# Kernel tuning notes

Measured on AMD Instinct MI355X. Metric: run time of the kernel, lower is better.

The kernel has to match this reference:

```python
import jax, jax.numpy as jnp
import numpy as np

B, H, L, DK, DV = 4, 16, 1024, 64, 64

def setup_inputs() -> dict:
    key = jax.random.key(0)
    k1, k2, k3, k4 = jax.random.split(key, 4)
    Q = jax.random.normal(k1, (B, H, L, DK), dtype=jnp.float32)
    K = jax.random.normal(k2, (B, H, L, DK), dtype=jnp.float32)
    V = jax.random.normal(k3, (B, H, L, DV), dtype=jnp.float32)
    attn_mask = jax.random.randint(k4, (B, H, L, L), 0, 2).astype(jnp.bool_)
    return {"Q": Q, "K": K, "V": V, "attn_mask": attn_mask}

def reference(Q, K, V, attn_mask):
    # NOTE: original torch code uses d_k = Q.size(1) == n_heads (a bug kept for fidelity)
    scale = 1.0 / jnp.sqrt(jnp.asarray(Q.shape[1], dtype=Q.dtype))
    scores = jnp.einsum('bhqd,bhkd->bhqk', Q, K) * scale
    scores = jnp.where(attn_mask, jnp.asarray(-1e9, dtype=scores.dtype), scores)
    attn = jax.nn.softmax(scores, axis=-1)
    context = jnp.einsum('bhqk,bhkv->bhqv', attn, V)
    return (context, attn)
```

## Files before the change

### kernel.cpp

```cpp
#include <hip/hip_runtime.h>
#include <hip/hip_bf16.h>

typedef _Float16 half8 __attribute__((ext_vector_type(8)));
typedef _Float16 half2v __attribute__((ext_vector_type(2)));
typedef __fp16 fp16x2 __attribute__((ext_vector_type(2)));
typedef float f32x4 __attribute__((ext_vector_type(4)));
typedef int i32x4 __attribute__((ext_vector_type(4)));

#define BH_ 64
#define L_ 1024
#define DK_ 64

__device__ __forceinline__ unsigned short f2h(float f) {
    _Float16 h = (_Float16)f;
    return __builtin_bit_cast(unsigned short, h);
}
__device__ __forceinline__ unsigned int pk2h(float a, float b) {
    fp16x2 h = __builtin_amdgcn_cvt_pkrtz(a, b);
    return __builtin_bit_cast(unsigned int, h);
}

template<int OFF>
__device__ __forceinline__ void gl_h8(half8& d, const unsigned short* p) {
    asm volatile("global_load_dwordx4 %0, %1, off offset:%2"
                 : "=&v"(d) : "v"(p), "n"(OFF));
}
template<int OFF>
__device__ __forceinline__ void gl_i4(i32x4& d, const int* p) {
    asm volatile("global_load_dwordx4 %0, %1, off offset:%2"
                 : "=&v"(d) : "v"(p), "n"(OFF));
}
template<int OFF>
__device__ __forceinline__ void gl_f4(f32x4& d, const float* p) {
    asm volatile("global_load_dwordx4 %0, %1, off offset:%2"
                 : "=&v"(d) : "v"(p), "n"(OFF));
}
template<int N>
__device__ __forceinline__ void wait_vm() {
    asm volatile("s_waitcnt vmcnt(%0)" :: "n"(N) : "memory");
    __builtin_amdgcn_sched_barrier(0);
}

__global__ void prep_k(const float* __restrict__ K, unsigned short* __restrict__ Kh) {
    int idx = blockIdx.x * 256 + threadIdx.x;
    float4 v = reinterpret_cast<const float4*>(K)[idx];
    ushort4 o;
    o.x = f2h(v.x); o.y = f2h(v.y); o.z = f2h(v.z); o.w = f2h(v.w);
    reinterpret_cast<ushort4*>(Kh)[idx] = o;
}

__global__ void prep_v(const float* __restrict__ V, unsigned short* __restrict__ Vt) {
    __shared__ float lds[64][65];
    int bh = blockIdx.x >> 4, kt = blockIdx.x & 15;
    int t = threadIdx.x;
    const float* Vb = V + ((size_t)bh * L_ + kt * 64) * DK_;
#pragma unroll
    for (int it = 0; it < 4; ++it) {
        int idx = it * 256 + t;
        int row = idx >> 4, c4 = idx & 15;
        float4 v = reinterpret_cast<const float4*>(Vb + (size_t)row * DK_)[c4];
        lds[row][c4 * 4 + 0] = v.x; lds[row][c4 * 4 + 1] = v.y;
        lds[row][c4 * 4 + 2] = v.z; lds[row][c4 * 4 + 3] = v.w;
    }
    __syncthreads();
    unsigned short* Vtb = Vt + (size_t)bh * 64 * L_ + kt * 64;
#pragma unroll
    for (int it = 0; it < 4; ++it) {
        int idx = it * 256 + t;
        int n = idx >> 4, c4 = idx & 15;
        ushort4 o;
        o.x = f2h(lds[c4 * 4 + 0][n]);
        o.y = f2h(lds[c4 * 4 + 1][n]);
        o.z = f2h(lds[c4 * 4 + 2][n]);
        o.w = f2h(lds[c4 * 4 + 3][n]);
        *reinterpret_cast<ushort4*>(Vtb + (size_t)n * L_ + c4 * 4) = o;
    }
}

__global__ __launch_bounds__(256, 3) void attn_main(
    const float* __restrict__ Q, const int* __restrict__ mask,
    const unsigned short* __restrict__ Kh, const unsigned short* __restrict__ Vt,
    float* __restrict__ ctx_out, float* __restrict__ attn_out)
{
    const int qt = blockIdx.x, bh = blockIdx.y;
    const int tid = threadIdx.x;
    const int w = tid >> 6;
    const int lane = tid & 63;
    const int lg = lane >> 4, lr = lane & 15;
    const int q0 = qt * 16;

    __shared__ float red[2][4][16];
    __shared__ union {
        unsigned short pbuf[4][640];
        float ctxbuf[4][16][68];
    } u;

    const size_t rowbase = ((size_t)bh * L_ + q0 + lr) * L_;
    const float* qp = Q + ((size_t)bh * L_ + q0 + lr) * DK_ + lg * 8;
    const int* mp = mask + rowbase + w * 256 + lg * 4;
    const unsigned short* kp = Kh + ((size_t)bh * L_ + w * 256 + lr) * DK_ + lg * 8;

    i32x4 mreg[16];
#define LM(T) gl_i4<(T) * 64>(mreg[T], mp)
    LM(0); LM(1); LM(2); LM(3); LM(4); LM(5); LM(6); LM(7);
    LM(8); LM(9); LM(10); LM(11); LM(12); LM(13); LM(14); LM(15);
#undef LM
    f32x4 qf0, qf1, qf2, qf3;
    gl_f4<0>(qf0, qp); gl_f4<16>(qf1, qp);
    gl_f4<128>(qf2, qp); gl_f4<144>(qf3, qp);

    half8 ka[2][4], kb[2][4];
#define ISSUE_K(BUF, C) { \
    const unsigned short* a0_ = kp + (C) * 4096; \
    const unsigned short* a2_ = a0_ + 2048; \
    gl_h8<0>(ka[BUF][0], a0_);    gl_h8<64>(kb[BUF][0], a0_); \
    gl_h8<2048>(ka[BUF][1], a0_); gl_h8<2112>(kb[BUF][1], a0_); \
    gl_h8<0>(ka[BUF][2], a2_);    gl_h8<64>(kb[BUF][2], a2_); \
    gl_h8<2048>(ka[BUF][3], a2_); gl_h8<2112>(kb[BUF][3], a2_); }
    ISSUE_K(0, 0);

    wait_vm<12>();
    unsigned int mw0 = 0, mw1 = 0;
#pragma unroll
    for (int t = 0; t < 8; ++t) {
        mw0 |= (unsigned(mreg[t][0] != 0) << (t * 4 + 0))
             | (unsigned(mreg[t][1] != 0) << (t * 4 + 1))
             | (unsigned(mreg[t][2] != 0) << (t * 4 + 2))
             | (unsigned(mreg[t][3] != 0) << (t * 4 + 3));
        mw1 |= (unsigned(mreg[t + 8][0] != 0) << (t * 4 + 0))
             | (unsigned(mreg[t + 8][1] != 0) << (t * 4 + 1))
             | (unsigned(mreg[t + 8][2] != 0) << (t * 4 + 2))
             | (unsigned(mreg[t + 8][3] != 0) << (t * 4 + 3));
    }

    wait_vm<8>();
    half8 qh[2];
#pragma unroll
    for (int j = 0; j < 4; ++j) {
        qh[0][j]     = (_Float16)qf0[j];
        qh[0][j + 4] = (_Float16)qf1[j];
        qh[1][j]     = (_Float16)qf2[j];
        qh[1][j + 4] = (_Float16)qf3[j];
    }

    ISSUE_K(1, 1);

    unsigned int sh[16][2];
    float mx = -INFINITY;
#define QK_TILE(BUF, T, TT) { \
    f32x4 acc_ = {0.f, 0.f, 0.f, 0.f}; \
    acc_ = __builtin_amdgcn_mfma_f32_16x16x32_f16(ka[BUF][T], qh[0], acc_, 0, 0, 0); \
    acc_ = __builtin_amdgcn_mfma_f32_16x16x32_f16(kb[BUF][T], qh[1], acc_, 0, 0, 0); \
    const unsigned int word_ = ((TT) < 8) ? mw0 : mw1; \
    float s0_ = ((word_ >> (((TT) & 7) * 4 + 0)) & 1u) ? -INFINITY : 0.25f * acc_[0]; \
    float s1_ = ((word_ >> (((TT) & 7) * 4 + 1)) & 1u) ? -INFINITY : 0.25f * acc_[1]; \
    float s2_ = ((word_ >> (((TT) & 7) * 4 + 2)) & 1u) ? -INFINITY : 0.25f * acc_[2]; \
    float s3_ = ((word_ >> (((TT) & 7) * 4 + 3)) & 1u) ? -INFINITY : 0.25f * acc_[3]; \
    sh[TT][0] = pk2h(s0_, s1_); sh[TT][1] = pk2h(s2_, s3_); \
    mx = fmaxf(mx, fmaxf(fmaxf(s0_, s1_), fmaxf(s2_, s3_))); }

    wait_vm<8>();
    QK_TILE(0, 0, 0); QK_TILE(0, 1, 1); QK_TILE(0, 2, 2); QK_TILE(0, 3, 3);
    ISSUE_K(0, 2);
    wait_vm<8>();
    QK_TILE(1, 0, 4); QK_TILE(1, 1, 5); QK_TILE(1, 2, 6); QK_TILE(1, 3, 7);
    ISSUE_K(1, 3);
    wait_vm<8>();
    QK_TILE(0, 0, 8); QK_TILE(0, 1, 9); QK_TILE(0, 2, 10); QK_TILE(0, 3, 11);
    wait_vm<0>();
    QK_TILE(1, 0, 12); QK_TILE(1, 1, 13); QK_TILE(1, 2, 14); QK_TILE(1, 3, 15);

    mx = fmaxf(mx, __shfl_xor(mx, 16));
    mx = fmaxf(mx, __shfl_xor(mx, 32));
    if (lane < 16) red[0][w][lr] = mx;
    __syncthreads();
    const float gm = fmaxf(fmaxf(red[0][0][lr], red[0][1][lr]),
                           fmaxf(red[0][2][lr], red[0][3][lr]));

    float lsum = 0.f;
#pragma unroll
    for (int tt = 0; tt < 16; ++tt) {
        half2v a = __builtin_bit_cast(half2v, sh[tt][0]);
        half2v b = __builtin_bit_cast(half2v, sh[tt][1]);
        float p0 = __expf((float)a[0] - gm);
        float p1 = __expf((float)a[1] - gm);
        float p2 = __expf((float)b[0] - gm);
        float p3 = __expf((float)b[1] - gm);
        lsum += (p0 + p1) + (p2 + p3);
        sh[tt][0] = pk2h(p0, p1);
        sh[tt][1] = pk2h(p2, p3);
    }
    lsum += __shfl_xor(lsum, 16);
    lsum += __shfl_xor(lsum, 32);
    if (lane < 16) red[1][w][lr] = lsum;
    __syncthreads();
    const float gsum = red[1][0][lr] + red[1][1][lr] + red[1][2][lr] + red[1][3][lr];
    const float rinv = 1.0f / gsum;

    const unsigned short* vp = Vt + ((size_t)bh * 64 + lr) * L_ + w * 256 + lg * 8;
    f32x4 cacc[4] = {{0,0,0,0},{0,0,0,0},{0,0,0,0},{0,0,0,0}};
    unsigned short* pb = &u.pbuf[w][0];
    half8 vv[2][2][4];
#define ISSUE_V(BUF, C) { \
    const unsigned short* b0_ = vp + (C) * 32; \
    const unsigned short* b1_ = b0_ + 16384; \
    const unsigned short* b2_ = b0_ + 32768; \
    const unsigned short* b3_ = b0_ + 49152; \
    gl_h8<0>(vv[BUF][0][0], b0_); gl_h8<64>(vv[BUF][1][0], b0_); \
    gl_h8<0>(vv[BUF][0][1], b1_); gl_h8<64>(vv[BUF][1][1], b1_); \
    gl_h8<0>(vv[BUF][0][2], b2_); gl_h8<64>(vv[BUF][1][2], b2_); \
    gl_h8<0>(vv[BUF][0][3], b3_); gl_h8<64>(vv[BUF][1][3], b3_); }
#define PV_C(BUF, H, C) { \
    uint2 pr0_; pr0_.x = sh[2 * (C)][0]; pr0_.y = sh[2 * (C)][1]; \
    *reinterpret_cast<uint2*>(&pb[lr * 40 + lg * 4]) = pr0_; \
    uint2 pr1_; pr1_.x = sh[2 * (C) + 1][0]; pr1_.y = sh[2 * (C) + 1][1]; \
    *reinterpret_cast<uint2*>(&pb[lr * 40 + 16 + lg * 4]) = pr1_; \
    half8 pa_ = *reinterpret_cast<const half8*>(&pb[lr * 40 + lg * 8]); \
    cacc[0] = __builtin_amdgcn_mfma_f32_16x16x32_f16(pa_, vv[BUF][H][0], cacc[0], 0, 0, 0); \
    cacc[1] = __builtin_amdgcn_mfma_f32_16x16x32_f16(pa_, vv[BUF][H][1], cacc[1], 0, 0, 0); \
    cacc[2] = __builtin_amdgcn_mfma_f32_16x16x32_f16(pa_, vv[BUF][H][2], cacc[2], 0, 0, 0); \
    cacc[3] = __builtin_amdgcn_mfma_f32_16x16x32_f16(pa_, vv[BUF][H][3], cacc[3], 0, 0, 0); }

    ISSUE_V(0, 0); ISSUE_V(1, 2);
    wait_vm<8>();  PV_C(0, 0, 0); PV_C(0, 1, 1); ISSUE_V(0, 4);
    wait_vm<8>();  PV_C(1, 0, 2); PV_C(1, 1, 3); ISSUE_V(1, 6);
    wait_vm<8>();  PV_C(0, 0, 4); PV_C(0, 1, 5);
    wait_vm<0>();  PV_C(1, 0, 6); PV_C(1, 1, 7);

#pragma unroll
    for (int tt = 0; tt < 16; ++tt) {
        half2v a = __builtin_bit_cast(half2v, sh[tt][0]);
        half2v b = __builtin_bit_cast(half2v, sh[tt][1]);
        float4 av;
        av.x = (float)a[0] * rinv; av.y = (float)a[1] * rinv;
        av.z = (float)b[0] * rinv; av.w = (float)b[1] * rinv;
        *reinterpret_cast<float4*>(&attn_out[rowbase + w * 256 + tt * 16 + lg * 4]) = av;
    }

    __syncthreads();
#pragma unroll
    for (int nt = 0; nt < 4; ++nt)
#pragma unroll
        for (int r = 0; r < 4; ++r)
            u.ctxbuf[w][lg * 4 + r][nt * 16 + lr] = cacc[nt][r];
    __syncthreads();
    {
        int e = tid * 4;
        int q = e >> 6, n = e & 63;
        float gs = red[1][0][q] + red[1][1][q] + red[1][2][q] + red[1][3][q];
        float rq = 1.0f / gs;
        float4 a0 = *reinterpret_cast<float4*>(&u.ctxbuf[0][q][n]);
        float4 a1 = *reinterpret_cast<float4*>(&u.ctxbuf[1][q][n]);
        float4 a2 = *reinterpret_cast<float4*>(&u.ctxbuf[2][q][n]);
        float4 a3 = *reinterpret_cast<float4*>(&u.ctxbuf[3][q][n]);
        float4 o;
        o.x = (a0.x + a1.x + a2.x + a3.x) * rq;
        o.y = (a0.y + a1.y + a2.y + a3.y) * rq;
        o.z = (a0.z + a1.z + a2.z + a3.z) * rq;
        o.w = (a0.w + a1.w + a2.w + a3.w) * rq;
        *reinterpret_cast<float4*>(&ctx_out[((size_t)bh * L_ + q0 + q) * DK_ + n]) = o;
    }
}

extern "C" void kernel_launch(void* const* d_in, const int* in_sizes, int n_in,
                              void* d_out, int out_size, void* d_ws, size_t ws_size,
                              hipStream_t stream) {
    const float* Q = (const float*)d_in[0];
    const float* K = (const float*)d_in[1];
    const float* V = (const float*)d_in[2];
    const int* mask = (const int*)d_in[3];
    float* ctx_out = (float*)d_out;
    float* attn_out = ctx_out + (size_t)BH_ * L_ * DK_;

    unsigned short* Kh = (unsigned short*)d_ws;
    unsigned short* Vt = Kh + (size_t)BH_ * L_ * DK_;

    hipLaunchKernelGGL(prep_k, dim3(4096), dim3(256), 0, stream, K, Kh);
    hipLaunchKernelGGL(prep_v, dim3(1024), dim3(256), 0, stream, V, Vt);
    hipLaunchKernelGGL(attn_main, dim3(64, 64), dim3(256), 0, stream,
                       Q, mask, Kh, Vt, ctx_out, attn_out);
}
```

Measured before the change: 212.2 us.

## Shrink prefetch buffers and stage mask loads to raise occupancy to four waves

Raises the launch-bounds occupancy hint from 3 to 4 blocks per CU. To fit the tighter register budget it cuts the mask register array from 16 to 8 vectors, the K double-buffer from 4 to 2 tiles per stage, and the V buffer from 2x2x4 to 2x4 half8s. Mask loads are staged in two halves interleaved with the QK tiles, and the load/compute pipelines run in finer steps with more waits. The aim is more waves per CU to hide memory latency, at the cost of less prefetch depth per wave and more wait points.

```diff
diff --git a/kernel.cpp b/kernel.cpp
--- a/kernel.cpp
+++ b/kernel.cpp
@@ -77,7 +77,7 @@
     }
 }
 
-__global__ __launch_bounds__(256, 3) void attn_main(
+__global__ __launch_bounds__(256, 4) void attn_main(
     const float* __restrict__ Q, const int* __restrict__ mask,
     const unsigned short* __restrict__ Kh, const unsigned short* __restrict__ Vt,
     float* __restrict__ ctx_out, float* __restrict__ attn_out)
@@ -100,39 +100,40 @@
     const int* mp = mask + rowbase + w * 256 + lg * 4;
     const unsigned short* kp = Kh + ((size_t)bh * L_ + w * 256 + lr) * DK_ + lg * 8;
 
-    i32x4 mreg[16];
-#define LM(T) gl_i4<(T) * 64>(mreg[T], mp)
-    LM(0); LM(1); LM(2); LM(3); LM(4); LM(5); LM(6); LM(7);
-    LM(8); LM(9); LM(10); LM(11); LM(12); LM(13); LM(14); LM(15);
-#undef LM
+    i32x4 mreg[8];
+    half8 ka[2][2], kb[2][2];
+#define ISSUE_K2(BUF, C) { \
+    const unsigned short* a_ = kp + (C) * 2048; \
+    gl_h8<0>(ka[BUF][0], a_);    gl_h8<64>(kb[BUF][0], a_); \
+    gl_h8<2048>(ka[BUF][1], a_); gl_h8<2112>(kb[BUF][1], a_); }
+#define ISSUE_M4(IDX, T) { \
+    gl_i4<(T) * 64 + 0>(mreg[(IDX) + 0], mp); \
+    gl_i4<(T) * 64 + 64>(mreg[(IDX) + 1], mp); \
+    gl_i4<(T) * 64 + 128>(mreg[(IDX) + 2], mp); \
+    gl_i4<(T) * 64 + 192>(mreg[(IDX) + 3], mp); }
+#define PACK_M4(DST, IDX) { \
+    DST = 0; \
+    _Pragma("unroll") \
+    for (int t = 0; t < 4; ++t) \
+        DST |= (unsigned(mreg[(IDX) + t][0] != 0) << (t * 4 + 0)) \
+             | (unsigned(mreg[(IDX) + t][1] != 0) << (t * 4 + 1)) \
+             | (unsigned(mreg[(IDX) + t][2] != 0) << (t * 4 + 2)) \
+             | (unsigned(mreg[(IDX) + t][3] != 0) << (t * 4 + 3)); }
+
+    ISSUE_M4(0, 0);
+    ISSUE_M4(4, 4);
     f32x4 qf0, qf1, qf2, qf3;
     gl_f4<0>(qf0, qp); gl_f4<16>(qf1, qp);
     gl_f4<128>(qf2, qp); gl_f4<144>(qf3, qp);
-
-    half8 ka[2][4], kb[2][4];
-#define ISSUE_K(BUF, C) { \
-    const unsigned short* a0_ = kp + (C) * 4096; \
-    const unsigned short* a2_ = a0_ + 2048; \
-    gl_h8<0>(ka[BUF][0], a0_);    gl_h8<64>(kb[BUF][0], a0_); \
-    gl_h8<2048>(ka[BUF][1], a0_); gl_h8<2112>(kb[BUF][1], a0_); \
-    gl_h8<0>(ka[BUF][2], a2_);    gl_h8<64>(kb[BUF][2], a2_); \
-    gl_h8<2048>(ka[BUF][3], a2_); gl_h8<2112>(kb[BUF][3], a2_); }
-    ISSUE_K(0, 0);
-
+    ISSUE_K2(0, 0);
+    ISSUE_K2(1, 1);
+
+    unsigned int mwA, mwB, mwC, mwD, mw0, mw1;
+    wait_vm<16>();
+    PACK_M4(mwA, 0);
     wait_vm<12>();
-    unsigned int mw0 = 0, mw1 = 0;
-#pragma unroll
-    for (int t = 0; t < 8; ++t) {
-        mw0 |= (unsigned(mreg[t][0] != 0) << (t * 4 + 0))
-             | (unsigned(mreg[t][1] != 0) << (t * 4 + 1))
-             | (unsigned(mreg[t][2] != 0) << (t * 4 + 2))
-             | (unsigned(mreg[t][3] != 0) << (t * 4 + 3));
-        mw1 |= (unsigned(mreg[t + 8][0] != 0) << (t * 4 + 0))
-             | (unsigned(mreg[t + 8][1] != 0) << (t * 4 + 1))
-             | (unsigned(mreg[t + 8][2] != 0) << (t * 4 + 2))
-             | (unsigned(mreg[t + 8][3] != 0) << (t * 4 + 3));
-    }
-
+    PACK_M4(mwB, 4);
+    mw0 = mwA | (mwB << 16);
     wait_vm<8>();
     half8 qh[2];
 #pragma unroll
@@ -143,32 +144,50 @@
         qh[1][j + 4] = (_Float16)qf3[j];
     }
 
-    ISSUE_K(1, 1);
-
     unsigned int sh[16][2];
     float mx = -INFINITY;
-#define QK_TILE(BUF, T, TT) { \
+#define QK_TILE(BUF, T, TT, WORD) { \
     f32x4 acc_ = {0.f, 0.f, 0.f, 0.f}; \
     acc_ = __builtin_amdgcn_mfma_f32_16x16x32_f16(ka[BUF][T], qh[0], acc_, 0, 0, 0); \
     acc_ = __builtin_amdgcn_mfma_f32_16x16x32_f16(kb[BUF][T], qh[1], acc_, 0, 0, 0); \
-    const unsigned int word_ = ((TT) < 8) ? mw0 : mw1; \
-    float s0_ = ((word_ >> (((TT) & 7) * 4 + 0)) & 1u) ? -INFINITY : 0.25f * acc_[0]; \
-    float s1_ = ((word_ >> (((TT) & 7) * 4 + 1)) & 1u) ? -INFINITY : 0.25f * acc_[1]; \
-    float s2_ = ((word_ >> (((TT) & 7) * 4 + 2)) & 1u) ? -INFINITY : 0.25f * acc_[2]; \
-    float s3_ = ((word_ >> (((TT) & 7) * 4 + 3)) & 1u) ? -INFINITY : 0.25f * acc_[3]; \
+    float s0_ = (((WORD) >> (((TT) & 7) * 4 + 0)) & 1u) ? -INFINITY : 0.25f * acc_[0]; \
+    float s1_ = (((WORD) >> (((TT) & 7) * 4 + 1)) & 1u) ? -INFINITY : 0.25f * acc_[1]; \
+    float s2_ = (((WORD) >> (((TT) & 7) * 4 + 2)) & 1u) ? -INFINITY : 0.25f * acc_[2]; \
+    float s3_ = (((WORD) >> (((TT) & 7) * 4 + 3)) & 1u) ? -INFINITY : 0.25f * acc_[3]; \
     sh[TT][0] = pk2h(s0_, s1_); sh[TT][1] = pk2h(s2_, s3_); \
     mx = fmaxf(mx, fmaxf(fmaxf(s0_, s1_), fmaxf(s2_, s3_))); }
-
+#define QK2(BUF, TT0, WORD) { \
+    QK_TILE(BUF, 0, TT0, WORD); QK_TILE(BUF, 1, (TT0) + 1, WORD); }
+
+    wait_vm<4>();
+    QK2(0, 0, mw0);
+    ISSUE_K2(0, 2);
+    wait_vm<4>();
+    QK2(1, 2, mw0);
+    ISSUE_M4(0, 8);
+    ISSUE_K2(1, 3);
     wait_vm<8>();
-    QK_TILE(0, 0, 0); QK_TILE(0, 1, 1); QK_TILE(0, 2, 2); QK_TILE(0, 3, 3);
-    ISSUE_K(0, 2);
+    QK2(0, 4, mw0);
+    ISSUE_M4(4, 12);
+    ISSUE_K2(0, 4);
+    wait_vm<12>();
+    PACK_M4(mwC, 0);
     wait_vm<8>();
-    QK_TILE(1, 0, 4); QK_TILE(1, 1, 5); QK_TILE(1, 2, 6); QK_TILE(1, 3, 7);
-    ISSUE_K(1, 3);
+    QK2(1, 6, mw0);
+    ISSUE_K2(1, 5);
     wait_vm<8>();
-    QK_TILE(0, 0, 8); QK_TILE(0, 1, 9); QK_TILE(0, 2, 10); QK_TILE(0, 3, 11);
+    PACK_M4(mwD, 4);
+    mw1 = mwC | (mwD << 16);
+    wait_vm<4>();
+    QK2(0, 8, mw1);
+    ISSUE_K2(0, 6);
+    wait_vm<4>();
+    QK2(1, 10, mw1);
+    ISSUE_K2(1, 7);
+    wait_vm<4>();
+    QK2(0, 12, mw1);
     wait_vm<0>();
-    QK_TILE(1, 0, 12); QK_TILE(1, 1, 13); QK_TILE(1, 2, 14); QK_TILE(1, 3, 15);
+    QK2(1, 14, mw1);
 
     mx = fmaxf(mx, __shfl_xor(mx, 16));
     mx = fmaxf(mx, __shfl_xor(mx, 32));
@@ -198,34 +217,36 @@
     const float rinv = 1.0f / gsum;
 
     const unsigned short* vp = Vt + ((size_t)bh * 64 + lr) * L_ + w * 256 + lg * 8;
+    const unsigned short* vp0 = vp;
+    const unsigned short* vp1 = vp + 16384;
+    const unsigned short* vp2 = vp + 32768;
+    const unsigned short* vp3 = vp + 49152;
     f32x4 cacc[4] = {{0,0,0,0},{0,0,0,0},{0,0,0,0},{0,0,0,0}};
     unsigned short* pb = &u.pbuf[w][0];
-    half8 vv[2][2][4];
-#define ISSUE_V(BUF, C) { \
-    const unsigned short* b0_ = vp + (C) * 32; \
-    const unsigned short* b1_ = b0_ + 16384; \
-    const unsigned short* b2_ = b0_ + 32768; \
-    const unsigned short* b3_ = b0_ + 49152; \
-    gl_h8<0>(vv[BUF][0][0], b0_); gl_h8<64>(vv[BUF][1][0], b0_); \
-    gl_h8<0>(vv[BUF][0][1], b1_); gl_h8<64>(vv[BUF][1][1], b1_); \
-    gl_h8<0>(vv[BUF][0][2], b2_); gl_h8<64>(vv[BUF][1][2], b2_); \
-    gl_h8<0>(vv[BUF][0][3], b3_); gl_h8<64>(vv[BUF][1][3], b3_); }
-#define PV_C(BUF, H, C) { \
+    half8 vv[2][4];
+#define ISSUE_V1(BUF, C) { \
+    gl_h8<(C) * 64>(vv[BUF][0], vp0); gl_h8<(C) * 64>(vv[BUF][1], vp1); \
+    gl_h8<(C) * 64>(vv[BUF][2], vp2); gl_h8<(C) * 64>(vv[BUF][3], vp3); }
+#define PV_C(BUF, C) { \
     uint2 pr0_; pr0_.x = sh[2 * (C)][0]; pr0_.y = sh[2 * (C)][1]; \
     *reinterpret_cast<uint2*>(&pb[lr * 40 + lg * 4]) = pr0_; \
     uint2 pr1_; pr1_.x = sh[2 * (C) + 1][0]; pr1_.y = sh[2 * (C) + 1][1]; \
     *reinterpret_cast<uint2*>(&pb[lr * 40 + 16 + lg * 4]) = pr1_; \
     half8 pa_ = *reinterpret_cast<const half8*>(&pb[lr * 40 + lg * 8]); \
-    cacc[0] = __builtin_amdgcn_mfma_f32_16x16x32_f16(pa_, vv[BUF][H][0], cacc[0], 0, 0, 0); \
-    cacc[1] = __builtin_amdgcn_mfma_f32_16x16x32_f16(pa_, vv[BUF][H][1], cacc[1], 0, 0, 0); \
-    cacc[2] = __builtin_amdgcn_mfma_f32_16x16x32_f16(pa_, vv[BUF][H][2], cacc[2], 0, 0, 0); \
-    cacc[3] = __builtin_amdgcn_mfma_f32_16x16x32_f16(pa_, vv[BUF][H][3], cacc[3], 0, 0, 0); }
-
-    ISSUE_V(0, 0); ISSUE_V(1, 2);
-    wait_vm<8>();  PV_C(0, 0, 0); PV_C(0, 1, 1); ISSUE_V(0, 4);
-    wait_vm<8>();  PV_C(1, 0, 2); PV_C(1, 1, 3); ISSUE_V(1, 6);
-    wait_vm<8>();  PV_C(0, 0, 4); PV_C(0, 1, 5);
-    wait_vm<0>();  PV_C(1, 0, 6); PV_C(1, 1, 7);
+    cacc[0] = __builtin_amdgcn_mfma_f32_16x16x32_f16(pa_, vv[BUF][0], cacc[0], 0, 0, 0); \
+    cacc[1] = __builtin_amdgcn_mfma_f32_16x16x32_f16(pa_, vv[BUF][1], cacc[1], 0, 0, 0); \
+    cacc[2] = __builtin_amdgcn_mfma_f32_16x16x32_f16(pa_, vv[BUF][2], cacc[2], 0, 0, 0); \
+    cacc[3] = __builtin_amdgcn_mfma_f32_16x16x32_f16(pa_, vv[BUF][3], cacc[3], 0, 0, 0); }
+
+    ISSUE_V1(0, 0); ISSUE_V1(1, 1);
+    wait_vm<4>(); PV_C(0, 0); ISSUE_V1(0, 2);
+    wait_vm<4>(); PV_C(1, 1); ISSUE_V1(1, 3);
+    wait_vm<4>(); PV_C(0, 2); ISSUE_V1(0, 4);
+    wait_vm<4>(); PV_C(1, 3); ISSUE_V1(1, 5);
+    wait_vm<4>(); PV_C(0, 4); ISSUE_V1(0, 6);
+    wait_vm<4>(); PV_C(1, 5); ISSUE_V1(1, 7);
+    wait_vm<4>(); PV_C(0, 6);
+    wait_vm<0>(); PV_C(1, 7);
 
 #pragma unroll
     for (int tt = 0; tt < 16; ++tt) {
```

Measured after the change: 226.8 us. +6.9%, slower.
